# Optimization experiments

Measured on AMD Instinct MI355X. Metric: run time of the kernel, lower is better.

Reference implementation:

```python
import jax, jax.numpy as jnp
import numpy as np

N = 50000       # nodes
E = 800000      # directed edges (before self-loops)
F_IN = 128      # dataset.num_features
HID = 16        # hidden per head (layer 1)
HEADS = 8
CLASSES = 16    # dataset.num_classes
NEG_SLOPE = 0.2 # GATConv default LeakyReLU slope


def setup_inputs() -> dict:
    key = jax.random.key(0)
    ks = jax.random.split(key, 10)
    s = 0.1  # glorot-ish scale for weights
    x = jax.random.normal(ks[0], (N, F_IN), jnp.float32)
    edge_index = jax.random.randint(ks[1], (2, E), 0, N, jnp.int32)
    W1 = jax.random.normal(ks[2], (F_IN, HEADS * HID), jnp.float32) * s
    a_src1 = jax.random.normal(ks[3], (HEADS, HID), jnp.float32) * s
    a_dst1 = jax.random.normal(ks[4], (HEADS, HID), jnp.float32) * s
    b1 = jnp.zeros((HEADS * HID,), jnp.float32)
    W2 = jax.random.normal(ks[5], (HEADS * HID, CLASSES), jnp.float32) * s
    a_src2 = jax.random.normal(ks[6], (1, CLASSES), jnp.float32) * s
    a_dst2 = jax.random.normal(ks[7], (1, CLASSES), jnp.float32) * s
    b2 = jnp.zeros((CLASSES,), jnp.float32)
    return {"x": x, "edge_index": edge_index, "W1": W1, "a_src1": a_src1,
            "a_dst1": a_dst1, "b1": b1, "W2": W2, "a_src2": a_src2,
            "a_dst2": a_dst2, "b2": b2}


def gat_conv(x, src, dst, W, a_s, a_d, b, concat):
    """PyG GATConv (eval mode): linear -> per-edge LeakyReLU attention ->
    per-destination segment softmax -> scatter-add aggregation."""
    n = x.shape[0]
    H, C = a_s.shape
    h = (x @ W).reshape(n, H, C)                       # [N,H,C]
    alpha_src = jnp.einsum('nhc,hc->nh', h, a_s)       # [N,H]
    alpha_dst = jnp.einsum('nhc,hc->nh', h, a_d)
    e = jax.nn.leaky_relu(alpha_src[src] + alpha_dst[dst], NEG_SLOPE)  # [E,H]
    # numerically stable segment softmax over incoming edges of each dst node
    emax = jax.ops.segment_max(e, dst, num_segments=n)
    emax = jnp.where(jnp.isfinite(emax), emax, 0.0)
    ex = jnp.exp(e - emax[dst])
    denom = jax.ops.segment_sum(ex, dst, num_segments=n)
    alpha = ex / (denom[dst] + 1e-16)                  # [E,H]
    out = jax.ops.segment_sum(alpha[:, :, None] * h[src], dst, num_segments=n)
    out = out.reshape(n, H * C) if concat else out.mean(axis=1)
    return out + b


def reference(x, edge_index, W1, a_src1, a_dst1, b1, W2, a_src2, a_dst2, b2):
    n = x.shape[0]
    loop = jnp.arange(n, dtype=edge_index.dtype)       # GATConv add_self_loops=True
    src = jnp.concatenate([edge_index[0], loop])
    dst = jnp.concatenate([edge_index[1], loop])
    # dropout layers are identity in eval mode
    h = jax.nn.elu(gat_conv(x, src, dst, W1, a_src1, a_dst1, b1, concat=True))
    out = gat_conv(h, src, dst, W2, a_src2, a_dst2, b2, concat=False)
    return out
```

## Files before the change

### kernel.cpp

```cpp
#include <hip/hip_runtime.h>
#include <hip/hip_bf16.h>
#include <math.h>

#define NN 50000
#define NE 800000
#define NBK 196
#define BCAP 5120
#define CHUNK 8192
#define NCH ((NE + CHUNK - 1) / CHUNK)
#define APITCH 136
#define G1BLOCKS ((NN + 63) / 64)

typedef short bf16x8 __attribute__((ext_vector_type(8)));
typedef float f32x4  __attribute__((ext_vector_type(4)));
typedef float f32x2  __attribute__((ext_vector_type(2)));

__device__ __forceinline__ unsigned short f2bf(float f) {
    union { float f; unsigned int i; } v; v.f = f;
    unsigned int x = v.i;
    unsigned int r = (x >> 16) & 1u;
    x += 0x7fffu + r;
    return (unsigned short)(x >> 16);
}
__device__ __forceinline__ void un2(unsigned int u, float& a, float& b) {
    union { unsigned int i; float f; } x, y;
    x.i = u << 16; y.i = u & 0xffff0000u;
    a = x.f; b = y.f;
}
__device__ __forceinline__ f32x2 up2(unsigned int u) {
    union { unsigned int i; float f; } x, y;
    x.i = u << 16; y.i = u & 0xffff0000u;
    return (f32x2){x.f, y.f};
}

__global__ __launch_bounds__(256) void k_swizw(const float* __restrict__ W1,
                                               uint4* __restrict__ W1s,
                                               int* __restrict__ gcur) {
    int t = threadIdx.x;
    if (blockIdx.x == 0 && t < NBK) gcur[t] = 0;
    int f = blockIdx.x * 256 + t;
    int nt = f >> 8, kc = (f >> 6) & 3, l = f & 63;
    int n  = nt * 16 + (l & 15);
    int k0 = kc * 32 + (l >> 4) * 8;
    unsigned int p[4];
#pragma unroll
    for (int jj = 0; jj < 4; jj++) {
        float v0 = W1[(k0 + 2 * jj) * 128 + n];
        float v1 = W1[(k0 + 2 * jj + 1) * 128 + n];
        p[jj] = (unsigned int)f2bf(v0) | ((unsigned int)f2bf(v1) << 16);
    }
    W1s[f] = make_uint4(p[0], p[1], p[2], p[3]);
}

__global__ __launch_bounds__(256) void k_bin_gemm1(
    const int* __restrict__ ei, int* __restrict__ gcur,
    unsigned int* __restrict__ packed,
    const float* __restrict__ x, const uint4* __restrict__ W1s,
    const float* __restrict__ aS, const float* __restrict__ aD,
    unsigned short* __restrict__ h1, float* __restrict__ as1,
    float* __restrict__ ad1)
{
    __shared__ union {
        struct { int h[NBK]; int bas[NBK]; } bin;
        unsigned short alds[64 * APITCH];
    } sm;
    int t = threadIdx.x;

    if (blockIdx.x < NCH) {
        int* h = sm.bin.h;
        int* bas = sm.bin.bas;
        if (t < NBK) h[t] = 0;
        __syncthreads();
        int cb = blockIdx.x * CHUNK;
#pragma unroll
        for (int k = 0; k < CHUNK / 256; k++) {
            int i = cb + k * 256 + t;
            if (i < NE) atomicAdd(&h[ei[NE + i] >> 8], 1);
        }
        __syncthreads();
        if (t < NBK) {
            int c = h[t];
            bas[t] = c ? (t * BCAP + atomicAdd(&gcur[t], c)) : 0;
            h[t] = 0;
        }
        __syncthreads();
#pragma unroll
        for (int k = 0; k < CHUNK / 256; k++) {
            int i = cb + k * 256 + t;
            if (i < NE) {
                int s = ei[i], d = ei[NE + i];
                int b = d >> 8;
                int r = atomicAdd(&h[b], 1);
                packed[bas[b] + r] = (unsigned int)s | ((unsigned int)(d & 255) << 16);
            }
        }
        return;
    }

    unsigned short* Alds = sm.alds;
    int w = t >> 6, l = t & 63;
    int rowbase = (blockIdx.x - NCH) * 64;

    {
        const float4* xg = (const float4*)(x + (size_t)rowbase * 128);
#pragma unroll
        for (int i = 0; i < 8; i++) {
            int idx = t + 256 * i;
            int r = idx >> 5, c = (idx & 31) * 4;
            float4 v = make_float4(0.f, 0.f, 0.f, 0.f);
            if (rowbase + r < NN) v = xg[idx];
            unsigned int p0 = (unsigned int)f2bf(v.x) | ((unsigned int)f2bf(v.y) << 16);
            unsigned int p1 = (unsigned int)f2bf(v.z) | ((unsigned int)f2bf(v.w) << 16);
            *(uint2*)&Alds[r * APITCH + c] = make_uint2(p0, p1);
        }
    }

    union BU { uint4 u; bf16x8 v; };
    BU b[2][4];
#pragma unroll
    for (int j = 0; j < 2; j++) {
        int nt = 2 * w + j;
#pragma unroll
        for (int kc = 0; kc < 4; kc++)
            b[j][kc].u = W1s[(nt * 4 + kc) * 64 + l];
    }
    __syncthreads();

    f32x4 acc[4][2];
#pragma unroll
    for (int mt = 0; mt < 4; mt++)
#pragma unroll
        for (int j = 0; j < 2; j++) acc[mt][j] = (f32x4){0.f, 0.f, 0.f, 0.f};

    int mrow = l & 15, quad = l >> 4;
#pragma unroll
    for (int kc = 0; kc < 4; kc++) {
#pragma unroll
        for (int mt = 0; mt < 4; mt++) {
            bf16x8 a = *(const bf16x8*)&Alds[(mt * 16 + mrow) * APITCH + kc * 32 + quad * 8];
            acc[mt][0] = __builtin_amdgcn_mfma_f32_16x16x32_bf16(a, b[0][kc].v, acc[mt][0], 0, 0, 0);
            acc[mt][1] = __builtin_amdgcn_mfma_f32_16x16x32_bf16(a, b[1][kc].v, acc[mt][1], 0, 0, 0);
        }
    }

#pragma unroll
    for (int j = 0; j < 2; j++) {
        int head = 2 * w + j;
        float aSv = aS[head * 16 + mrow];
        float aDv = aD[head * 16 + mrow];
#pragma unroll
        for (int mt = 0; mt < 4; mt++) {
#pragma unroll
            for (int reg = 0; reg < 4; reg++) {
                float s = acc[mt][j][reg] * aSv;
                float d = acc[mt][j][reg] * aDv;
                s += __shfl_xor(s, 1); s += __shfl_xor(s, 2);
                s += __shfl_xor(s, 4); s += __shfl_xor(s, 8);
                d += __shfl_xor(d, 1); d += __shfl_xor(d, 2);
                d += __shfl_xor(d, 4); d += __shfl_xor(d, 8);
                if (mrow == 0) {
                    int grow = rowbase + mt * 16 + quad * 4 + reg;
                    if (grow < NN) {
                        as1[grow * 8 + head] = s;
                        ad1[grow * 8 + head] = d;
                    }
                }
            }
        }
    }

    __syncthreads();
#pragma unroll
    for (int mt = 0; mt < 4; mt++)
#pragma unroll
        for (int j = 0; j < 2; j++) {
            int col = w * 32 + j * 16 + mrow;
#pragma unroll
            for (int reg = 0; reg < 4; reg++) {
                int r = mt * 16 + quad * 4 + reg;
                Alds[r * APITCH + col] = f2bf(acc[mt][j][reg]);
            }
        }
    __syncthreads();
    uint4* hg = (uint4*)h1;
#pragma unroll
    for (int i = 0; i < 4; i++) {
        int idx = t + 256 * i;
        int r = idx >> 4, ci = idx & 15;
        if (rowbase + r < NN)
            hg[(size_t)(rowbase + r) * 16 + ci] = *(const uint4*)&Alds[r * APITCH + ci * 8];
    }
}

__global__ __launch_bounds__(256) void k_final(const unsigned int* __restrict__ packed,
                                               const int* __restrict__ gcur,
                                               int* __restrict__ deg,
                                               int* __restrict__ offs,
                                               int* __restrict__ ssrc) {
    __shared__ unsigned int pk[BCAP + 64];
    __shared__ int osl[BCAP + 64];
    __shared__ int cnt[256], pre[256], cur[256];
    int t = threadIdx.x, b = blockIdx.x;
    int start = b * BCAP;
    int n = gcur[b];
    for (int i = t; i < n; i += 256) pk[i] = packed[start + i];
    cnt[t] = 0;
    __syncthreads();
    for (int i = t; i < n; i += 256) atomicAdd(&cnt[(pk[i] >> 16) & 255], 1);
    __syncthreads();
    int v = cnt[t];
    pre[t] = v;
    __syncthreads();
    for (int off = 1; off < 256; off <<= 1) {
        int u = (t >= off) ? pre[t - off] : 0;
        __syncthreads();
        pre[t] += u;
        __syncthreads();
    }
    int excl = pre[t] - v;
    int dst = b * 256 + t;
    if (dst < NN) { deg[dst] = v; offs[dst] = start + excl; }
    cur[t] = excl;
    __syncthreads();
    for (int i = t; i < n; i += 256) {
        unsigned int p = pk[i];
        int r = atomicAdd(&cur[(p >> 16) & 255], 1);
        osl[r] = (int)(p & 0xffffu);
    }
    __syncthreads();
    for (int i = t; i < n; i += 256) ssrc[start + i] = osl[i];
}

__global__ __launch_bounds__(256) void k_agg1(
    const int* __restrict__ offs, const int* __restrict__ deg,
    const int* __restrict__ ssrc,
    const float* __restrict__ as1, const float* __restrict__ ad1,
    const unsigned short* __restrict__ h1, const float* __restrict__ b1,
    unsigned short* __restrict__ h2)
{
    int wave = threadIdx.x >> 6;
    int lane = threadIdx.x & 63;
    int node = blockIdx.x * 4 + wave;
    if (node >= NN) return;
    int start = offs[node], cnt = deg[node];

    int li = lane & 7, jg = lane >> 3;
    float adv = ad1[node * 8 + li];

    const uint4* h1u4 = (const uint4*)h1;
    f32x2 acc[8];
#pragma unroll
    for (int i = 0; i < 8; i++) acc[i] = (f32x2){0.f, 0.f};
    float dsum = 0.f;

    for (int base = 0; base <= cnt; base += 32) {
#pragma unroll
        for (int u = 0; u < 4; u++) {
            int j = base + u * 8 + jg;
            if (j <= cnt) {
                int s = (j < cnt) ? ssrc[start + j] : node;
                float e = as1[s * 8 + li] + adv;
                e = (e > 0.f) ? e : 0.2f * e;
                float w = __expf(e);
                uint4 ha = h1u4[(size_t)s * 16 + 2 * li];
                uint4 hb = h1u4[(size_t)s * 16 + 2 * li + 1];
                f32x2 w2 = (f32x2){w, w};
                acc[0] += w2 * up2(ha.x); acc[1] += w2 * up2(ha.y);
                acc[2] += w2 * up2(ha.z); acc[3] += w2 * up2(ha.w);
                acc[4] += w2 * up2(hb.x); acc[5] += w2 * up2(hb.y);
                acc[6] += w2 * up2(hb.z); acc[7] += w2 * up2(hb.w);
                dsum += w;
            }
        }
    }

#pragma unroll
    for (int i = 0; i < 8; i++) {
        acc[i].x += __shfl_xor(acc[i].x, 8);  acc[i].y += __shfl_xor(acc[i].y, 8);
        acc[i].x += __shfl_xor(acc[i].x, 16); acc[i].y += __shfl_xor(acc[i].y, 16);
        acc[i].x += __shfl_xor(acc[i].x, 32); acc[i].y += __shfl_xor(acc[i].y, 32);
    }
    dsum += __shfl_xor(dsum, 8);
    dsum += __shfl_xor(dsum, 16);
    dsum += __shfl_xor(dsum, 32);

    if (jg == 0) {
        float inv = 1.0f / dsum;
        int c0 = li * 16;
        float v[16];
#pragma unroll
        for (int i = 0; i < 8; i++) {
            float v0 = acc[i].x * inv + b1[c0 + 2 * i];
            float v1 = acc[i].y * inv + b1[c0 + 2 * i + 1];
            v[2 * i]     = (v0 > 0.f) ? v0 : (__expf(v0) - 1.0f);
            v[2 * i + 1] = (v1 > 0.f) ? v1 : (__expf(v1) - 1.0f);
        }
        uint4 o0, o1;
        o0.x = (unsigned int)f2bf(v[0])  | ((unsigned int)f2bf(v[1])  << 16);
        o0.y = (unsigned int)f2bf(v[2])  | ((unsigned int)f2bf(v[3])  << 16);
        o0.z = (unsigned int)f2bf(v[4])  | ((unsigned int)f2bf(v[5])  << 16);
        o0.w = (unsigned int)f2bf(v[6])  | ((unsigned int)f2bf(v[7])  << 16);
        o1.x = (unsigned int)f2bf(v[8])  | ((unsigned int)f2bf(v[9])  << 16);
        o1.y = (unsigned int)f2bf(v[10]) | ((unsigned int)f2bf(v[11]) << 16);
        o1.z = (unsigned int)f2bf(v[12]) | ((unsigned int)f2bf(v[13]) << 16);
        o1.w = (unsigned int)f2bf(v[14]) | ((unsigned int)f2bf(v[15]) << 16);
        ((uint4*)h2)[(size_t)node * 16 + 2 * li] = o0;
        ((uint4*)h2)[(size_t)node * 16 + 2 * li + 1] = o1;
    }
}

__global__ __launch_bounds__(256) void k_gemm2(
    const unsigned short* __restrict__ h2,
    const float* __restrict__ W2,
    const float* __restrict__ aS2,
    const float* __restrict__ aD2,
    float* __restrict__ g2,
    float* __restrict__ as2, float* __restrict__ ad2)
{
    __shared__ float Wl[128 * 16];
    __shared__ float xl[32 * 129];
    __shared__ float aSf[16], aDf[16];
    int t = threadIdx.x;

    for (int i = t; i < 2048; i += 256) Wl[i] = W2[i];
    if (t < 16) { aSf[t] = aS2[t]; aDf[t] = aD2[t]; }

    int rowbase = blockIdx.x * 32;
    for (int i = t; i < 2048; i += 256) {
        int row = rowbase + (i >> 6);
        unsigned int u = (row < NN) ? ((const unsigned int*)h2)[(size_t)rowbase * 64 + i] : 0u;
        float a, b; un2(u, a, b);
        int lin = 2 * i;
        int rr = lin >> 7, kk = lin & 127;
        xl[rr * 129 + kk] = a;
        xl[rr * 129 + kk + 1] = b;
    }
    __syncthreads();

    int r = t >> 3, cp = t & 7;
    int row = rowbase + r;
    float a0 = 0.f, a1 = 0.f;
    const float* xrow = &xl[r * 129];
#pragma unroll 4
    for (int k = 0; k < 128; k++) {
        float xv = xrow[k];
        a0 += xv * Wl[k * 16 + 2 * cp];
        a1 += xv * Wl[k * 16 + 2 * cp + 1];
    }
    if (row < NN) ((float2*)g2)[(size_t)row * 8 + cp] = make_float2(a0, a1);

    float asp = a0 * aSf[2 * cp] + a1 * aSf[2 * cp + 1];
    float adp = a0 * aDf[2 * cp] + a1 * aDf[2 * cp + 1];
    asp += __shfl_xor(asp, 1); asp += __shfl_xor(asp, 2); asp += __shfl_xor(asp, 4);
    adp += __shfl_xor(adp, 1); adp += __shfl_xor(adp, 2); adp += __shfl_xor(adp, 4);
    if (cp == 0 && row < NN) { as2[row] = asp; ad2[row] = adp; }
}

__global__ __launch_bounds__(256) void k_agg2(
    const int* __restrict__ offs, const int* __restrict__ deg,
    const int* __restrict__ ssrc,
    const float* __restrict__ as2, const float* __restrict__ ad2,
    const float* __restrict__ g2, const float* __restrict__ b2,
    float* __restrict__ out)
{
    int wave = threadIdx.x >> 6;
    int lane = threadIdx.x & 63;
    int node = blockIdx.x * 4 + wave;
    if (node >= NN) return;
    int start = offs[node], cnt = deg[node];
    float adv = ad2[node];

    int li4 = lane & 3, jg = lane >> 2;
    const float4* g2f4 = (const float4*)g2;

    float a0 = 0.f, a1 = 0.f, a2 = 0.f, a3 = 0.f, dsum = 0.f;
    for (int base = 0; base <= cnt; base += 32) {
#pragma unroll
        for (int u = 0; u < 2; u++) {
            int j = base + u * 16 + jg;
            if (j <= cnt) {
                int s = (j < cnt) ? ssrc[start + j] : node;
                float e = as2[s] + adv;
                e = (e > 0.f) ? e : 0.2f * e;
                float w = __expf(e);
                float4 g = g2f4[(size_t)s * 4 + li4];
                a0 += w * g.x; a1 += w * g.y; a2 += w * g.z; a3 += w * g.w;
                if (li4 == 0) dsum += w;
            }
        }
    }
#pragma unroll
    for (int m = 4; m < 64; m <<= 1) {
        a0 += __shfl_xor(a0, m); a1 += __shfl_xor(a1, m);
        a2 += __shfl_xor(a2, m); a3 += __shfl_xor(a3, m);
        dsum += __shfl_xor(dsum, m);
    }
    dsum += __shfl_xor(dsum, 1);
    dsum += __shfl_xor(dsum, 2);

    if (jg == 0) {
        float inv = 1.0f / dsum;
        const float4* b2f4 = (const float4*)b2;
        float4 bb = b2f4[li4];
        float4 o = make_float4(a0 * inv + bb.x, a1 * inv + bb.y,
                               a2 * inv + bb.z, a3 * inv + bb.w);
        ((float4*)out)[(size_t)node * 4 + li4] = o;
    }
}

extern "C" void kernel_launch(void* const* d_in, const int* in_sizes, int n_in,
                              void* d_out, int out_size, void* d_ws, size_t ws_size,
                              hipStream_t stream) {
    const float* x   = (const float*)d_in[0];
    const int*   ei  = (const int*)d_in[1];
    const float* W1  = (const float*)d_in[2];
    const float* aS1 = (const float*)d_in[3];
    const float* aD1 = (const float*)d_in[4];
    const float* b1  = (const float*)d_in[5];
    const float* W2  = (const float*)d_in[6];
    const float* aS2 = (const float*)d_in[7];
    const float* aD2 = (const float*)d_in[8];
    const float* b2  = (const float*)d_in[9];

    char* ws = (char*)d_ws;
    size_t off = 0;
    auto alloc = [&](size_t bytes) { void* p = ws + off; off += (bytes + 255) & ~(size_t)255; return p; };

    unsigned short* h1 = (unsigned short*)alloc((size_t)NN * 128 * 2);
    unsigned short* h2 = (unsigned short*)alloc((size_t)NN * 128 * 2);
    float* as1 = (float*)alloc((size_t)NN * 8 * 4);
    float* ad1 = (float*)alloc((size_t)NN * 8 * 4);
    float* g2  = (float*)alloc((size_t)NN * 16 * 4);
    float* as2 = (float*)alloc((size_t)NN * 4);
    float* ad2 = (float*)alloc((size_t)NN * 4);
    int* deg    = (int*)alloc((size_t)NN * 4);
    int* offs   = (int*)alloc((size_t)NN * 4);
    int* ssrc   = (int*)alloc((size_t)NBK * BCAP * 4);
    unsigned int* packed = (unsigned int*)alloc((size_t)NBK * BCAP * 4);
    int* gcur   = (int*)alloc((size_t)NBK * 4);
    uint4* W1s  = (uint4*)alloc((size_t)2048 * 16);

    k_swizw<<<8, 256, 0, stream>>>(W1, W1s, gcur);
    k_bin_gemm1<<<NCH + G1BLOCKS, 256, 0, stream>>>(ei, gcur, packed,
                                                    x, W1s, aS1, aD1, h1, as1, ad1);
    k_final<<<NBK, 256, 0, stream>>>(packed, gcur, deg, offs, ssrc);
    k_agg1<<<(NN + 3) / 4, 256, 0, stream>>>(offs, deg, ssrc, as1, ad1, h1, b1, h2);
    k_gemm2<<<(NN + 31) / 32, 256, 0, stream>>>(h2, W2, aS2, aD2, g2, as2, ad2);
    k_agg2<<<(NN + 3) / 4, 256, 0, stream>>>(offs, deg, ssrc, as2, ad2, g2, b2,
                                             (float*)d_out);
}
```

Before: 199.2 us.

## Use bf16 MFMA for layer-2 GEMM and fold self-loops into CSR

The layer-2 projection now runs on bf16 MFMA (16x16x32) instead of a scalar FP32 LDS loop. W2 is pre-swizzled into MFMA B-fragment layout by an extra block of the weight-swizzle kernel. The bucket-finalize kernel now writes each node's self-loop into the sorted source list and bumps its degree, so both aggregation kernels drop the per-edge special case for the self-loop. This trades some precision in the layer-2 GEMM inputs for less scalar ALU and LDS traffic. Shared buffers are tighter and assume each bucket's edges plus its 256 self-loops fit within BCAP.

```diff
diff --git a/kernel.cpp b/kernel.cpp
--- a/kernel.cpp
+++ b/kernel.cpp
@@ -34,10 +34,25 @@
 }
 
 __global__ __launch_bounds__(256) void k_swizw(const float* __restrict__ W1,
+                                               const float* __restrict__ W2,
                                                uint4* __restrict__ W1s,
+                                               uint4* __restrict__ W2s,
                                                int* __restrict__ gcur) {
     int t = threadIdx.x;
-    if (blockIdx.x == 0 && t < NBK) gcur[t] = 0;
+    if (blockIdx.x == 8) {
+        if (t < NBK) gcur[t] = 0;
+        int kc = t >> 6, l = t & 63;
+        int n = l & 15, k0 = kc * 32 + (l >> 4) * 8;
+        unsigned int p[4];
+#pragma unroll
+        for (int jj = 0; jj < 4; jj++) {
+            float v0 = W2[(k0 + 2 * jj) * 16 + n];
+            float v1 = W2[(k0 + 2 * jj + 1) * 16 + n];
+            p[jj] = (unsigned int)f2bf(v0) | ((unsigned int)f2bf(v1) << 16);
+        }
+        W2s[t] = make_uint4(p[0], p[1], p[2], p[3]);
+        return;
+    }
     int f = blockIdx.x * 256 + t;
     int nt = f >> 8, kc = (f >> 6) & 3, l = f & 63;
     int n  = nt * 16 + (l & 15);
@@ -197,12 +212,13 @@
                                                int* __restrict__ deg,
                                                int* __restrict__ offs,
                                                int* __restrict__ ssrc) {
-    __shared__ unsigned int pk[BCAP + 64];
-    __shared__ int osl[BCAP + 64];
+    __shared__ unsigned int pk[BCAP];
+    __shared__ int osl[BCAP];
     __shared__ int cnt[256], pre[256], cur[256];
     int t = threadIdx.x, b = blockIdx.x;
     int start = b * BCAP;
     int n = gcur[b];
+    int nnodes = NN - b * 256; if (nnodes > 256) nnodes = 256;
     for (int i = t; i < n; i += 256) pk[i] = packed[start + i];
     cnt[t] = 0;
     __syncthreads();
@@ -218,9 +234,14 @@
         __syncthreads();
     }
     int excl = pre[t] - v;
+    int mybase = excl + t;
     int dst = b * 256 + t;
-    if (dst < NN) { deg[dst] = v; offs[dst] = start + excl; }
-    cur[t] = excl;
+    if (dst < NN) {
+        deg[dst] = v + 1;
+        offs[dst] = start + mybase;
+        osl[mybase + v] = dst;
+    }
+    cur[t] = mybase;
     __syncthreads();
     for (int i = t; i < n; i += 256) {
         unsigned int p = pk[i];
@@ -228,7 +249,8 @@
         osl[r] = (int)(p & 0xffffu);
     }
     __syncthreads();
-    for (int i = t; i < n; i += 256) ssrc[start + i] = osl[i];
+    int n2 = n + nnodes;
+    for (int i = t; i < n2; i += 256) ssrc[start + i] = osl[i];
 }
 
 __global__ __launch_bounds__(256) void k_agg1(
@@ -242,7 +264,7 @@
     int lane = threadIdx.x & 63;
     int node = blockIdx.x * 4 + wave;
     if (node >= NN) return;
-    int start = offs[node], cnt = deg[node];
+    int start = offs[node], cnt2 = deg[node];
 
     int li = lane & 7, jg = lane >> 3;
     float adv = ad1[node * 8 + li];
@@ -253,12 +275,12 @@
     for (int i = 0; i < 8; i++) acc[i] = (f32x2){0.f, 0.f};
     float dsum = 0.f;
 
-    for (int base = 0; base <= cnt; base += 32) {
+    for (int base = 0; base < cnt2; base += 32) {
 #pragma unroll
         for (int u = 0; u < 4; u++) {
             int j = base + u * 8 + jg;
-            if (j <= cnt) {
-                int s = (j < cnt) ? ssrc[start + j] : node;
+            if (j < cnt2) {
+                int s = ssrc[start + j];
                 float e = as1[s * 8 + li] + adv;
                 e = (e > 0.f) ? e : 0.2f * e;
                 float w = __expf(e);
@@ -311,49 +333,39 @@
 
 __global__ __launch_bounds__(256) void k_gemm2(
     const unsigned short* __restrict__ h2,
-    const float* __restrict__ W2,
-    const float* __restrict__ aS2,
-    const float* __restrict__ aD2,
-    float* __restrict__ g2,
-    float* __restrict__ as2, float* __restrict__ ad2)
+    const uint4* __restrict__ W2s,
+    const float* __restrict__ aS2, const float* __restrict__ aD2,
+    float* __restrict__ g2, float* __restrict__ as2, float* __restrict__ ad2)
 {
-    __shared__ float Wl[128 * 16];
-    __shared__ float xl[32 * 129];
-    __shared__ float aSf[16], aDf[16];
     int t = threadIdx.x;
-
-    for (int i = t; i < 2048; i += 256) Wl[i] = W2[i];
-    if (t < 16) { aSf[t] = aS2[t]; aDf[t] = aD2[t]; }
-
-    int rowbase = blockIdx.x * 32;
-    for (int i = t; i < 2048; i += 256) {
-        int row = rowbase + (i >> 6);
-        unsigned int u = (row < NN) ? ((const unsigned int*)h2)[(size_t)rowbase * 64 + i] : 0u;
-        float a, b; un2(u, a, b);
-        int lin = 2 * i;
-        int rr = lin >> 7, kk = lin & 127;
-        xl[rr * 129 + kk] = a;
-        xl[rr * 129 + kk + 1] = b;
-    }
-    __syncthreads();
-
-    int r = t >> 3, cp = t & 7;
-    int row = rowbase + r;
-    float a0 = 0.f, a1 = 0.f;
-    const float* xrow = &xl[r * 129];
-#pragma unroll 4
-    for (int k = 0; k < 128; k++) {
-        float xv = xrow[k];
-        a0 += xv * Wl[k * 16 + 2 * cp];
-        a1 += xv * Wl[k * 16 + 2 * cp + 1];
-    }
-    if (row < NN) ((float2*)g2)[(size_t)row * 8 + cp] = make_float2(a0, a1);
-
-    float asp = a0 * aSf[2 * cp] + a1 * aSf[2 * cp + 1];
-    float adp = a0 * aDf[2 * cp] + a1 * aDf[2 * cp + 1];
-    asp += __shfl_xor(asp, 1); asp += __shfl_xor(asp, 2); asp += __shfl_xor(asp, 4);
-    adp += __shfl_xor(adp, 1); adp += __shfl_xor(adp, 2); adp += __shfl_xor(adp, 4);
-    if (cp == 0 && row < NN) { as2[row] = asp; ad2[row] = adp; }
+    int w = t >> 6, l = t & 63;
+    int rowbase = blockIdx.x * 64 + w * 16;
+    int arow = l & 15, quad = l >> 4;
+    int row = rowbase + arow; if (row >= NN) row = NN - 1;
+
+    union BU { uint4 u; bf16x8 v; };
+    f32x4 acc = (f32x4){0.f, 0.f, 0.f, 0.f};
+#pragma unroll
+    for (int kc = 0; kc < 4; kc++) {
+        bf16x8 a = *(const bf16x8*)&h2[(size_t)row * 128 + kc * 32 + quad * 8];
+        BU b; b.u = W2s[kc * 64 + l];
+        acc = __builtin_amdgcn_mfma_f32_16x16x32_bf16(a, b.v, acc, 0, 0, 0);
+    }
+
+    int col = l & 15;
+    float aSv = aS2[col], aDv = aD2[col];
+#pragma unroll
+    for (int reg = 0; reg < 4; reg++) {
+        int grow = rowbase + quad * 4 + reg;
+        if (grow < NN) g2[(size_t)grow * 16 + col] = acc[reg];
+        float s = acc[reg] * aSv;
+        float d = acc[reg] * aDv;
+        s += __shfl_xor(s, 1); s += __shfl_xor(s, 2);
+        s += __shfl_xor(s, 4); s += __shfl_xor(s, 8);
+        d += __shfl_xor(d, 1); d += __shfl_xor(d, 2);
+        d += __shfl_xor(d, 4); d += __shfl_xor(d, 8);
+        if (col == 0 && grow < NN) { as2[grow] = s; ad2[grow] = d; }
+    }
 }
 
 __global__ __launch_bounds__(256) void k_agg2(
@@ -367,19 +379,19 @@
     int lane = threadIdx.x & 63;
     int node = blockIdx.x * 4 + wave;
     if (node >= NN) return;
-    int start = offs[node], cnt = deg[node];
+    int start = offs[node], cnt2 = deg[node];
     float adv = ad2[node];
 
     int li4 = lane & 3, jg = lane >> 2;
     const float4* g2f4 = (const float4*)g2;
 
     float a0 = 0.f, a1 = 0.f, a2 = 0.f, a3 = 0.f, dsum = 0.f;
-    for (int base = 0; base <= cnt; base += 32) {
+    for (int base = 0; base < cnt2; base += 32) {
 #pragma unroll
         for (int u = 0; u < 2; u++) {
             int j = base + u * 16 + jg;
-            if (j <= cnt) {
-                int s = (j < cnt) ? ssrc[start + j] : node;
+            if (j < cnt2) {
+                int s = ssrc[start + j];
                 float e = as2[s] + adv;
                 e = (e > 0.f) ? e : 0.2f * e;
                 float w = __expf(e);
@@ -439,13 +451,14 @@
     unsigned int* packed = (unsigned int*)alloc((size_t)NBK * BCAP * 4);
     int* gcur   = (int*)alloc((size_t)NBK * 4);
     uint4* W1s  = (uint4*)alloc((size_t)2048 * 16);
-
-    k_swizw<<<8, 256, 0, stream>>>(W1, W1s, gcur);
+    uint4* W2s  = (uint4*)alloc((size_t)256 * 16);
+
+    k_swizw<<<9, 256, 0, stream>>>(W1, W2, W1s, W2s, gcur);
     k_bin_gemm1<<<NCH + G1BLOCKS, 256, 0, stream>>>(ei, gcur, packed,
                                                     x, W1s, aS1, aD1, h1, as1, ad1);
     k_final<<<NBK, 256, 0, stream>>>(packed, gcur, deg, offs, ssrc);
     k_agg1<<<(NN + 3) / 4, 256, 0, stream>>>(offs, deg, ssrc, as1, ad1, h1, b1, h2);
-    k_gemm2<<<(NN + 31) / 32, 256, 0, stream>>>(h2, W2, aS2, aD2, g2, as2, ad2);
+    k_gemm2<<<(NN + 63) / 64, 256, 0, stream>>>(h2, W2s, aS2, aD2, g2, as2, ad2);
     k_agg2<<<(NN + 3) / 4, 256, 0, stream>>>(offs, deg, ssrc, as2, ad2, g2, b2,
                                              (float*)d_out);
 }
```

Measured after the change: 188.8 us. 1.05x faster.
